# Kernel tuning notes

Hardware: AMD Instinct MI355X
Metric: run time of the kernel (lower is better)

Reference implementation:

```python
import jax, jax.numpy as jnp
import numpy as np

N_NODES = 100000
N_EDGES = 3200000
SIGMA_REF = 0.07
T_REF = 293.15
DSIGMA_DT = -0.0001
PHI_THRESH = 0.3
EPS = 1e-8


def compute_gradient(T, pos, edge_index):
    """Edge-based finite-difference gradient, scatter-reduced to nodes.

    grad_T[i] = mean over incoming edges (src->i) of
                (T[src]-T[i]) * (pos[src]-pos[i]) / |pos[src]-pos[i]|^2
    """
    src, dst = edge_index[0], edge_index[1]
    dT = T[src] - T[dst]                         # [E]
    dpos = pos[src] - pos[dst]                   # [E,3]
    dist2 = jnp.sum(dpos * dpos, axis=-1) + EPS  # [E]
    contrib = (dT / dist2)[:, None] * dpos       # [E,3]
    num = jax.ops.segment_sum(contrib, dst, num_segments=N_NODES)            # [N,3]
    cnt = jax.ops.segment_sum(jnp.ones_like(dT), dst, num_segments=N_NODES)  # [N]
    return num / jnp.maximum(cnt, 1.0)[:, None]


def setup_inputs() -> dict:
    key = jax.random.key(0)
    k1, k2, k3 = jax.random.split(key, 3)
    x = jax.random.normal(k1, (N_NODES, 9), dtype=jnp.float32)
    pos = jax.random.normal(k2, (N_NODES, 3), dtype=jnp.float32)
    edge_index = jax.random.randint(k3, (2, N_EDGES), 0, N_NODES, dtype=jnp.int64)
    return {"x": x, "pos": pos, "edge_index": edge_index}


def reference(x, pos, edge_index):
    T = x[:, 3]
    phi = x[:, 8]
    grad_T = compute_gradient(T, pos, edge_index)          # [N,3]
    force = DSIGMA_DT * grad_T                             # [N,3]
    interface_mask = (jnp.abs(phi) < PHI_THRESH).astype(force.dtype)
    return force * interface_mask[:, None]
```

## Files before the change

kernel.cpp:

```cpp
#include <hip/hip_runtime.h>

#define N_NODES 100000
#define N_EDGES 3200000
#define NVEC    (N_EDGES / 4)

#define S_LOG2  10
#define S       (1 << S_LOG2)
#define NPART   ((N_NODES + S - 1) / S)
#define NPITEMS 768
#define EMAX    5008

#define EPB     6252
#define NB      512
#define CAP     35000

constexpr float DSIGMA_DT  = -0.0001f;
constexpr float PHI_THRESH = 0.3f;
constexpr float EPS        = 1e-8f;

__global__ __launch_bounds__(512) void bin_kernel(const int4* __restrict__ ei4,
                                                  const float* __restrict__ x,
                                                  const float* __restrict__ pos,
                                                  float4* __restrict__ posT,
                                                  int* __restrict__ gcur,
                                                  int* __restrict__ buckets) {
    __shared__ int   lbuf[EPB];
    __shared__ unsigned short lrk[EPB];
    __shared__ unsigned char  lbinS[EPB];
    __shared__ int hist[NPART], lofs[NPART], baseg[NPART];
    const int tid = threadIdx.x;

    {
        const int per = (N_NODES + NB - 1) / NB;
        const int lo = blockIdx.x * per;
        const int hi = min(lo + per, N_NODES);
        for (int i = lo + tid; i < hi; i += 512)
            posT[i] = make_float4(pos[3 * i], pos[3 * i + 1], pos[3 * i + 2],
                                  x[9 * i + 3]);
    }

    const int ebase = blockIdx.x * EPB;
    const int n  = min(EPB, N_EDGES - ebase);
    const int nv = n >> 2;
    const int4* __restrict__ src4 = ei4 + (ebase >> 2);
    const int4* __restrict__ dst4 = ei4 + NVEC + (ebase >> 2);

    if (tid < NPART) hist[tid] = 0;
    __syncthreads();

    for (int v = tid; v < nv; v += 512) {
        int4 d = dst4[v];
#pragma unroll
        for (int k = 0; k < 4; ++k) {
            int dk = k == 0 ? d.x : k == 1 ? d.y : k == 2 ? d.z : d.w;
            int bin = dk >> S_LOG2;
            int rank = atomicAdd(&hist[bin], 1);
            lrk[4 * v + k] = (unsigned short)rank;
        }
    }
    __syncthreads();

    if (tid < 64) {
        int a = hist[tid];
        int b = (64 + tid < NPART) ? hist[64 + tid] : 0;
        int sa = a, sb = b;
#pragma unroll
        for (int d = 1; d < 64; d <<= 1) {
            int t = __shfl_up(sa, d, 64); if (tid >= d) sa += t;
            int u = __shfl_up(sb, d, 64); if (tid >= d) sb += u;
        }
        int tot_a = __shfl(sa, 63, 64);
        lofs[tid] = sa - a;
        if (64 + tid < NPART) lofs[64 + tid] = tot_a + sb - b;
    }
    __syncthreads();
    if (tid < NPART) baseg[tid] = atomicAdd(&gcur[tid], hist[tid]);
    __syncthreads();

    for (int v = tid; v < nv; v += 512) {
        int4 s = src4[v];
        int4 d = dst4[v];
#pragma unroll
        for (int k = 0; k < 4; ++k) {
            int dk = k == 0 ? d.x : k == 1 ? d.y : k == 2 ? d.z : d.w;
            int sk = k == 0 ? s.x : k == 1 ? s.y : k == 2 ? s.z : s.w;
            int bin = dk >> S_LOG2;
            int pos = lofs[bin] + (int)lrk[4 * v + k];
            lbuf[pos]  = (sk << S_LOG2) | (dk & (S - 1));
            lbinS[pos] = (unsigned char)bin;
        }
    }
    __syncthreads();

    for (int i = tid; i < n; i += 512) {
        int b   = lbinS[i];
        int pos = baseg[b] + (i - lofs[b]);
        if (pos < CAP) buckets[(size_t)b * CAP + pos] = lbuf[i];
    }
}

__global__ __launch_bounds__(512, 8) void part_kernel(
        const int* __restrict__ gcur,
        const int* __restrict__ buckets,
        const float4* __restrict__ posT,
        float4* __restrict__ partials) {
    __shared__ int S2[EMAX];
    __shared__ unsigned short RK[EMAX];
    __shared__ int hist[S];
    __shared__ int base[S];
    const int item = blockIdx.x, tid = threadIdx.x;
    const int p     = (item * NPART) / NPITEMS;
    const int first = (p * NPITEMS + NPART - 1) / NPART;
    const int next  = ((p + 1) * NPITEMS + NPART - 1) / NPART;
    const int ncp   = next - first;
    const int c     = item - first;
    const int lo = p << S_LOG2;

    for (int i = tid; i < S; i += 512) hist[i] = 0;

    const int len = min(gcur[p], CAP);
    const int beg = (int)((long long)len * c / ncp);
    const int end = (int)((long long)len * (c + 1) / ncp);
    const int nloc = end - beg;
    const int* __restrict__ bp = buckets + (size_t)p * CAP;
    __syncthreads();

    for (int i = tid; i < nloc; i += 512) {
        int v = bp[beg + i];
        RK[i] = (unsigned short)atomicAdd(&hist[v & (S - 1)], 1);
    }
    __syncthreads();

    if (tid < 64) {
        int carry = 0;
        for (int b = 0; b < S; b += 64) {
            int v = hist[b + tid];
            int orig = v;
#pragma unroll
            for (int d = 1; d < 64; d <<= 1) {
                int t = __shfl_up(v, d, 64);
                if (tid >= d) v += t;
            }
            base[b + tid] = carry + v - orig;
            carry += __shfl(v, 63, 64);
        }
    }
    __syncthreads();

    for (int i = tid; i < nloc; i += 512) {
        int v = bp[beg + i];
        S2[base[v & (S - 1)] + (int)RK[i]] = v >> S_LOG2;
    }
    __syncthreads();

    float4* __restrict__ outp = partials + ((size_t)item << S_LOG2);
    for (int r = tid; r < S; r += 512) {
        int nseg = hist[r];
        int node = lo + r;
        float4 b = (node < N_NODES && nseg > 0) ? posT[node]
                                                : make_float4(0.f, 0.f, 0.f, 0.f);
        float ax = 0.f, ay = 0.f, az = 0.f;
        int b0 = base[r];
        for (int j = b0; j < b0 + nseg; ++j) {
            float4 a = posT[S2[j]];
            float px = a.x - b.x, py = a.y - b.y, pz = a.z - b.z;
            float dT = a.w - b.w;
            float w  = dT / (px * px + py * py + pz * pz + EPS);
            ax += w * px; ay += w * py; az += w * pz;
        }
        outp[r] = make_float4(ax, ay, az, (float)nseg);
    }
}

__global__ void finalize_kernel(const float* __restrict__ x,
                                const float4* __restrict__ partials,
                                float* __restrict__ out) {
    int i = blockIdx.x * blockDim.x + threadIdx.x;
    if (i >= N_NODES) return;
    int p = i >> S_LOG2;
    int s = i & (S - 1);
    int first = (p * NPITEMS + NPART - 1) / NPART;
    int next  = ((p + 1) * NPITEMS + NPART - 1) / NPART;
    int ncp   = next - first;
    float ax = 0.f, ay = 0.f, az = 0.f, aw = 0.f;
#pragma unroll 8
    for (int c = 0; c < ncp; ++c) {
        float4 t = partials[(((size_t)(first + c)) << S_LOG2) + s];
        ax += t.x; ay += t.y; az += t.z; aw += t.w;
    }
    float phi = x[i * 9 + 8];
    float cn = aw > 1.0f ? aw : 1.0f;
    float m = (fabsf(phi) < PHI_THRESH) ? (DSIGMA_DT / cn) : 0.0f;
    out[3 * i]     = m * ax;
    out[3 * i + 1] = m * ay;
    out[3 * i + 2] = m * az;
}

__global__ void prep_kernel(const float* __restrict__ x,
                            const float* __restrict__ pos,
                            float4* __restrict__ posT) {
    int i = blockIdx.x * blockDim.x + threadIdx.x;
    if (i < N_NODES)
        posT[i] = make_float4(pos[3 * i], pos[3 * i + 1], pos[3 * i + 2],
                              x[9 * i + 3]);
}

__global__ void edge_scatter_atomic_kernel(const int* __restrict__ ei,
                                           const float4* __restrict__ posT,
                                           float4* __restrict__ accum) {
    int e = blockIdx.x * blockDim.x + threadIdx.x;
    if (e >= N_EDGES) return;
    int s = ei[e];
    int d = ei[N_EDGES + e];
    float4 a = posT[s];
    float4 b = posT[d];
    float px = a.x - b.x, py = a.y - b.y, pz = a.z - b.z;
    float dT = a.w - b.w;
    float w  = dT / (px * px + py * py + pz * pz + EPS);
    float* ac = (float*)&accum[d];
    atomicAdd(ac,     w * px);
    atomicAdd(ac + 1, w * py);
    atomicAdd(ac + 2, w * pz);
    atomicAdd(ac + 3, 1.0f);
}

__global__ void finalize_accum_kernel(const float* __restrict__ x,
                                      const float4* __restrict__ accum,
                                      float* __restrict__ out) {
    int i = blockIdx.x * blockDim.x + threadIdx.x;
    if (i >= N_NODES) return;
    float4 a = accum[i];
    float phi = x[i * 9 + 8];
    float cn = a.w > 1.0f ? a.w : 1.0f;
    float m = (fabsf(phi) < PHI_THRESH) ? (DSIGMA_DT / cn) : 0.0f;
    out[3 * i]     = m * a.x;
    out[3 * i + 1] = m * a.y;
    out[3 * i + 2] = m * a.z;
}

extern "C" void kernel_launch(void* const* d_in, const int* in_sizes, int n_in,
                              void* d_out, int out_size, void* d_ws, size_t ws_size,
                              hipStream_t stream) {
    const float* x   = (const float*)d_in[0];
    const float* pos = (const float*)d_in[1];
    const int*   ei  = (const int*)d_in[2];
    float* out = (float*)d_out;

    const size_t posT_b = (size_t)N_NODES * sizeof(float4);
    const size_t part_b = (size_t)NPITEMS * S * sizeof(float4);
    const size_t gcur_b = 512;
    const size_t buck_b = (size_t)NPART * CAP * sizeof(int);

    char* w = (char*)d_ws;
    float4* posT     = (float4*)w;
    float4* partials = (float4*)(w + posT_b);
    int*    gcur     = (int*)(w + posT_b + part_b);
    int*    buckets  = (int*)(w + posT_b + part_b + gcur_b);

    const size_t need_full = posT_b + part_b + gcur_b + buck_b;

    const int B = 256;

    if (ws_size >= need_full) {
        hipMemsetAsync(gcur, 0, gcur_b, stream);
        bin_kernel<<<NB, 512, 0, stream>>>((const int4*)ei, x, pos, posT, gcur, buckets);
        part_kernel<<<NPITEMS, 512, 0, stream>>>(gcur, buckets, posT, partials);
        finalize_kernel<<<(N_NODES + B - 1) / B, B, 0, stream>>>(x, partials, out);
    } else {
        float4* accum = (float4*)(w + posT_b);
        prep_kernel<<<(N_NODES + B - 1) / B, B, 0, stream>>>(x, pos, posT);
        hipMemsetAsync(accum, 0, (size_t)N_NODES * sizeof(float4), stream);
        edge_scatter_atomic_kernel<<<(N_EDGES + B - 1) / B, B, 0, stream>>>(ei, posT, accum);
        finalize_accum_kernel<<<(N_NODES + B - 1) / B, B, 0, stream>>>(x, accum, out);
    }
}
```

Baseline: 122.4 us.

## Replace per-partition counting sort with LDS float atomic accumulation

The partition kernel no longer counting-sorts edges by destination (histogram, prefix scan, scatter, then a per-node serial gather). Each edge is processed directly: it gathers the source position, reads the destination position from a cached LDS copy, and atomically adds its contribution and count into LDS accumulators. This removes two barriers, the scan and the imbalanced per-node serial loop, in exchange for four LDS atomics per edge, three of them float. The float atomics also make the summation order nondeterministic.

Measured after the change: 152.7 us. 24.8% more time.

```diff
diff --git a/kernel.cpp b/kernel.cpp
--- a/kernel.cpp
+++ b/kernel.cpp
@@ -8,7 +8,6 @@
 #define S       (1 << S_LOG2)
 #define NPART   ((N_NODES + S - 1) / S)
 #define NPITEMS 768
-#define EMAX    5008
 
 #define EPB     6252
 #define NB      512
@@ -104,10 +103,11 @@
         const int* __restrict__ buckets,
         const float4* __restrict__ posT,
         float4* __restrict__ partials) {
-    __shared__ int S2[EMAX];
-    __shared__ unsigned short RK[EMAX];
-    __shared__ int hist[S];
-    __shared__ int base[S];
+    __shared__ float  accx[S];
+    __shared__ float  accy[S];
+    __shared__ float  accz[S];
+    __shared__ int    hist[S];
+    __shared__ float4 ploc[S];
     const int item = blockIdx.x, tid = threadIdx.x;
     const int p     = (item * NPART) / NPITEMS;
     const int first = (p * NPITEMS + NPART - 1) / NPART;
@@ -116,7 +116,11 @@
     const int c     = item - first;
     const int lo = p << S_LOG2;
 
-    for (int i = tid; i < S; i += 512) hist[i] = 0;
+    for (int i = tid; i < S; i += 512) {
+        accx[i] = 0.f; accy[i] = 0.f; accz[i] = 0.f; hist[i] = 0;
+        int node = lo + i;
+        ploc[i] = (node < N_NODES) ? posT[node] : make_float4(0.f, 0.f, 0.f, 0.f);
+    }
 
     const int len = min(gcur[p], CAP);
     const int beg = (int)((long long)len * c / ncp);
@@ -127,49 +131,23 @@
 
     for (int i = tid; i < nloc; i += 512) {
         int v = bp[beg + i];
-        RK[i] = (unsigned short)atomicAdd(&hist[v & (S - 1)], 1);
-    }
-    __syncthreads();
-
-    if (tid < 64) {
-        int carry = 0;
-        for (int b = 0; b < S; b += 64) {
-            int v = hist[b + tid];
-            int orig = v;
-#pragma unroll
-            for (int d = 1; d < 64; d <<= 1) {
-                int t = __shfl_up(v, d, 64);
-                if (tid >= d) v += t;
-            }
-            base[b + tid] = carry + v - orig;
-            carry += __shfl(v, 63, 64);
-        }
-    }
-    __syncthreads();
-
-    for (int i = tid; i < nloc; i += 512) {
-        int v = bp[beg + i];
-        S2[base[v & (S - 1)] + (int)RK[i]] = v >> S_LOG2;
+        int d = v & (S - 1);
+        int s = v >> S_LOG2;
+        float4 a = posT[s];
+        float4 b = ploc[d];
+        float px = a.x - b.x, py = a.y - b.y, pz = a.z - b.z;
+        float dT = a.w - b.w;
+        float w  = dT / (px * px + py * py + pz * pz + EPS);
+        atomicAdd(&accx[d], w * px);
+        atomicAdd(&accy[d], w * py);
+        atomicAdd(&accz[d], w * pz);
+        atomicAdd(&hist[d], 1);
     }
     __syncthreads();
 
     float4* __restrict__ outp = partials + ((size_t)item << S_LOG2);
-    for (int r = tid; r < S; r += 512) {
-        int nseg = hist[r];
-        int node = lo + r;
-        float4 b = (node < N_NODES && nseg > 0) ? posT[node]
-                                                : make_float4(0.f, 0.f, 0.f, 0.f);
-        float ax = 0.f, ay = 0.f, az = 0.f;
-        int b0 = base[r];
-        for (int j = b0; j < b0 + nseg; ++j) {
-            float4 a = posT[S2[j]];
-            float px = a.x - b.x, py = a.y - b.y, pz = a.z - b.z;
-            float dT = a.w - b.w;
-            float w  = dT / (px * px + py * py + pz * pz + EPS);
-            ax += w * px; ay += w * py; az += w * pz;
-        }
-        outp[r] = make_float4(ax, ay, az, (float)nseg);
-    }
+    for (int r = tid; r < S; r += 512)
+        outp[r] = make_float4(accx[r], accy[r], accz[r], (float)hist[r]);
 }
 
 __global__ void finalize_kernel(const float* __restrict__ x,
```

## Use finer 128-node partitions and fuse finalize into the partition kernel

Applied to the files above, without the earlier changes.

Shrinks destination partitions from 1024 to 128 nodes, giving 782 buckets that each fit one block. This removes the split-partition partials buffer and the separate finalize kernel. Each block now sorts its bucket locally, has four lanes per node reduce edges with shuffles, and writes masked output directly. The cost is a heavier bin kernel: bigger histogram and scan, 16-bit bin ids, more global atomics, and more scattered bucket writes. Buckets are capped at 4992 edges, which the expected average of about 4096 per bucket should satisfy.

New measurement: 120.6 us. About the same (-1.4%).

```diff
diff --git a/kernel.cpp b/kernel.cpp
--- a/kernel.cpp
+++ b/kernel.cpp
@@ -4,15 +4,14 @@
 #define N_EDGES 3200000
 #define NVEC    (N_EDGES / 4)
 
-#define S_LOG2  10
+#define S_LOG2  7
 #define S       (1 << S_LOG2)
 #define NPART   ((N_NODES + S - 1) / S)
-#define NPITEMS 768
-#define EMAX    5008
+#define NPB     832
 
 #define EPB     6252
 #define NB      512
-#define CAP     35000
+#define CAP     4992
 
 constexpr float DSIGMA_DT  = -0.0001f;
 constexpr float PHI_THRESH = 0.3f;
@@ -26,8 +25,9 @@
                                                   int* __restrict__ buckets) {
     __shared__ int   lbuf[EPB];
     __shared__ unsigned short lrk[EPB];
-    __shared__ unsigned char  lbinS[EPB];
-    __shared__ int hist[NPART], lofs[NPART], baseg[NPART];
+    __shared__ unsigned short lbinS[EPB];
+    __shared__ int hist[NPB], lofs[NPB];
+    __shared__ int baseg[NPART];
     const int tid = threadIdx.x;
 
     {
@@ -45,7 +45,7 @@
     const int4* __restrict__ src4 = ei4 + (ebase >> 2);
     const int4* __restrict__ dst4 = ei4 + NVEC + (ebase >> 2);
 
-    if (tid < NPART) hist[tid] = 0;
+    for (int i = tid; i < NPB; i += 512) hist[i] = 0;
     __syncthreads();
 
     for (int v = tid; v < nv; v += 512) {
@@ -61,20 +61,22 @@
     __syncthreads();
 
     if (tid < 64) {
-        int a = hist[tid];
-        int b = (64 + tid < NPART) ? hist[64 + tid] : 0;
-        int sa = a, sb = b;
-#pragma unroll
-        for (int d = 1; d < 64; d <<= 1) {
-            int t = __shfl_up(sa, d, 64); if (tid >= d) sa += t;
-            int u = __shfl_up(sb, d, 64); if (tid >= d) sb += u;
-        }
-        int tot_a = __shfl(sa, 63, 64);
-        lofs[tid] = sa - a;
-        if (64 + tid < NPART) lofs[64 + tid] = tot_a + sb - b;
-    }
-    __syncthreads();
-    if (tid < NPART) baseg[tid] = atomicAdd(&gcur[tid], hist[tid]);
+        int carry = 0;
+        for (int b = 0; b < NPB; b += 64) {
+            int v = hist[b + tid];
+            int orig = v;
+#pragma unroll
+            for (int d = 1; d < 64; d <<= 1) {
+                int t = __shfl_up(v, d, 64);
+                if (tid >= d) v += t;
+            }
+            lofs[b + tid] = carry + v - orig;
+            carry += __shfl(v, 63, 64);
+        }
+    }
+    __syncthreads();
+    for (int i = tid; i < NPART; i += 512)
+        baseg[i] = atomicAdd(&gcur[i], hist[i]);
     __syncthreads();
 
     for (int v = tid; v < nv; v += 512) {
@@ -87,7 +89,7 @@
             int bin = dk >> S_LOG2;
             int pos = lofs[bin] + (int)lrk[4 * v + k];
             lbuf[pos]  = (sk << S_LOG2) | (dk & (S - 1));
-            lbinS[pos] = (unsigned char)bin;
+            lbinS[pos] = (unsigned short)bin;
         }
     }
     __syncthreads();
@@ -103,30 +105,26 @@
         const int* __restrict__ gcur,
         const int* __restrict__ buckets,
         const float4* __restrict__ posT,
-        float4* __restrict__ partials) {
-    __shared__ int S2[EMAX];
-    __shared__ unsigned short RK[EMAX];
-    __shared__ int hist[S];
-    __shared__ int base[S];
-    const int item = blockIdx.x, tid = threadIdx.x;
-    const int p     = (item * NPART) / NPITEMS;
-    const int first = (p * NPITEMS + NPART - 1) / NPART;
-    const int next  = ((p + 1) * NPITEMS + NPART - 1) / NPART;
-    const int ncp   = next - first;
-    const int c     = item - first;
+        const float* __restrict__ x,
+        float* __restrict__ out) {
+    __shared__ int S2[CAP];
+    __shared__ unsigned short RK[CAP];
+    __shared__ int hist[S], base[S];
+    __shared__ float4 ploc[S];
+    const int p = blockIdx.x, tid = threadIdx.x;
     const int lo = p << S_LOG2;
 
-    for (int i = tid; i < S; i += 512) hist[i] = 0;
-
+    if (tid < S) {
+        hist[tid] = 0;
+        int node = lo + tid;
+        ploc[tid] = (node < N_NODES) ? posT[node] : make_float4(0.f, 0.f, 0.f, 0.f);
+    }
     const int len = min(gcur[p], CAP);
-    const int beg = (int)((long long)len * c / ncp);
-    const int end = (int)((long long)len * (c + 1) / ncp);
-    const int nloc = end - beg;
     const int* __restrict__ bp = buckets + (size_t)p * CAP;
     __syncthreads();
 
-    for (int i = tid; i < nloc; i += 512) {
-        int v = bp[beg + i];
+    for (int i = tid; i < len; i += 512) {
+        int v = bp[i];
         RK[i] = (unsigned short)atomicAdd(&hist[v & (S - 1)], 1);
     }
     __syncthreads();
@@ -147,53 +145,36 @@
     }
     __syncthreads();
 
-    for (int i = tid; i < nloc; i += 512) {
-        int v = bp[beg + i];
+    for (int i = tid; i < len; i += 512) {
+        int v = bp[i];
         S2[base[v & (S - 1)] + (int)RK[i]] = v >> S_LOG2;
     }
     __syncthreads();
 
-    float4* __restrict__ outp = partials + ((size_t)item << S_LOG2);
-    for (int r = tid; r < S; r += 512) {
-        int nseg = hist[r];
-        int node = lo + r;
-        float4 b = (node < N_NODES && nseg > 0) ? posT[node]
-                                                : make_float4(0.f, 0.f, 0.f, 0.f);
-        float ax = 0.f, ay = 0.f, az = 0.f;
-        int b0 = base[r];
-        for (int j = b0; j < b0 + nseg; ++j) {
-            float4 a = posT[S2[j]];
-            float px = a.x - b.x, py = a.y - b.y, pz = a.z - b.z;
-            float dT = a.w - b.w;
-            float w  = dT / (px * px + py * py + pz * pz + EPS);
-            ax += w * px; ay += w * py; az += w * pz;
-        }
-        outp[r] = make_float4(ax, ay, az, (float)nseg);
-    }
-}
-
-__global__ void finalize_kernel(const float* __restrict__ x,
-                                const float4* __restrict__ partials,
-                                float* __restrict__ out) {
-    int i = blockIdx.x * blockDim.x + threadIdx.x;
-    if (i >= N_NODES) return;
-    int p = i >> S_LOG2;
-    int s = i & (S - 1);
-    int first = (p * NPITEMS + NPART - 1) / NPART;
-    int next  = ((p + 1) * NPITEMS + NPART - 1) / NPART;
-    int ncp   = next - first;
-    float ax = 0.f, ay = 0.f, az = 0.f, aw = 0.f;
-#pragma unroll 8
-    for (int c = 0; c < ncp; ++c) {
-        float4 t = partials[(((size_t)(first + c)) << S_LOG2) + s];
-        ax += t.x; ay += t.y; az += t.z; aw += t.w;
-    }
-    float phi = x[i * 9 + 8];
-    float cn = aw > 1.0f ? aw : 1.0f;
-    float m = (fabsf(phi) < PHI_THRESH) ? (DSIGMA_DT / cn) : 0.0f;
-    out[3 * i]     = m * ax;
-    out[3 * i + 1] = m * ay;
-    out[3 * i + 2] = m * az;
+    const int r = tid >> 2, q = tid & 3;
+    const int node = lo + r;
+    const int nseg = hist[r];
+    const int b0 = base[r];
+    float4 b = ploc[r];
+    float ax = 0.f, ay = 0.f, az = 0.f;
+    for (int j = b0 + q; j < b0 + nseg; j += 4) {
+        float4 a = posT[S2[j]];
+        float px = a.x - b.x, py = a.y - b.y, pz = a.z - b.z;
+        float dT = a.w - b.w;
+        float w  = dT / (px * px + py * py + pz * pz + EPS);
+        ax += w * px; ay += w * py; az += w * pz;
+    }
+    ax += __shfl_down(ax, 2, 64); ax += __shfl_down(ax, 1, 64);
+    ay += __shfl_down(ay, 2, 64); ay += __shfl_down(ay, 1, 64);
+    az += __shfl_down(az, 2, 64); az += __shfl_down(az, 1, 64);
+    if (q == 0 && node < N_NODES) {
+        float phi = x[node * 9 + 8];
+        float cn = nseg > 1 ? (float)nseg : 1.0f;
+        float m = (fabsf(phi) < PHI_THRESH) ? (DSIGMA_DT / cn) : 0.0f;
+        out[3 * node]     = m * ax;
+        out[3 * node + 1] = m * ay;
+        out[3 * node + 2] = m * az;
+    }
 }
 
 __global__ void prep_kernel(const float* __restrict__ x,
@@ -247,25 +228,22 @@
     float* out = (float*)d_out;
 
     const size_t posT_b = (size_t)N_NODES * sizeof(float4);
-    const size_t part_b = (size_t)NPITEMS * S * sizeof(float4);
-    const size_t gcur_b = 512;
+    const size_t gcur_b = 4096;
     const size_t buck_b = (size_t)NPART * CAP * sizeof(int);
 
     char* w = (char*)d_ws;
-    float4* posT     = (float4*)w;
-    float4* partials = (float4*)(w + posT_b);
-    int*    gcur     = (int*)(w + posT_b + part_b);
-    int*    buckets  = (int*)(w + posT_b + part_b + gcur_b);
-
-    const size_t need_full = posT_b + part_b + gcur_b + buck_b;
+    float4* posT    = (float4*)w;
+    int*    gcur    = (int*)(w + posT_b);
+    int*    buckets = (int*)(w + posT_b + gcur_b);
+
+    const size_t need_full = posT_b + gcur_b + buck_b;
 
     const int B = 256;
 
     if (ws_size >= need_full) {
         hipMemsetAsync(gcur, 0, gcur_b, stream);
         bin_kernel<<<NB, 512, 0, stream>>>((const int4*)ei, x, pos, posT, gcur, buckets);
-        part_kernel<<<NPITEMS, 512, 0, stream>>>(gcur, buckets, posT, partials);
-        finalize_kernel<<<(N_NODES + B - 1) / B, B, 0, stream>>>(x, partials, out);
+        part_kernel<<<NPART, 512, 0, stream>>>(gcur, buckets, posT, x, out);
     } else {
         float4* accum = (float4*)(w + posT_b);
         prep_kernel<<<(N_NODES + B - 1) / B, B, 0, stream>>>(x, pos, posT);
```
